# Kernel optimization log

Measured on AMD Instinct MI355X. Metric: run time of the kernel, lower is better.

The kernel has to match this reference:

```python
import jax, jax.numpy as jnp
import numpy as np

NUM_HEADS = 4


def _mha_pool(seg):
    """seg: [n_seg, S, H]. First 4 channels are attention logits (softmax over S),
    rest are values split into 4 heads; returns [n_seg, H-4]."""
    n_seg, S, H = seg.shape
    attn = jax.nn.softmax(seg[:, :, :NUM_HEADS], axis=1)          # [n, S, 4]
    vals = seg[:, :, NUM_HEADS:].reshape(n_seg, S, NUM_HEADS, -1)  # [n, S, 4, hd]
    pooled = jnp.einsum('nsh,nshd->nhd', attn, vals)               # [n, 4, hd]
    return pooled.reshape(n_seg, -1)


def setup_inputs() -> dict:
    key = jax.random.key(0)
    k1, k2, k3, k4 = jax.random.split(key, 4)
    T, D, H = 131072, 2048, 260
    embeddings = jax.random.normal(k1, (T, D), dtype=jnp.float32)
    labels = jax.random.randint(k2, (T,), 0, 2, dtype=jnp.int32)
    W_down = jax.random.normal(k3, (D, H), dtype=jnp.float32) / np.sqrt(D)
    b_down = jnp.zeros((H,), dtype=jnp.float32)
    W_final = jax.random.normal(k4, (H - NUM_HEADS, 1), dtype=jnp.float32) / np.sqrt(H - NUM_HEADS)
    b_final = jnp.zeros((1,), dtype=jnp.float32)
    return {
        'embeddings': embeddings,
        'W_down': W_down,
        'b_down': b_down,
        'W_final': W_final,
        'b_final': b_final,
        'labels': labels,
        'tokens_per_problem': 512,
        'tokens_per_line': 16,
    }


def reference(embeddings, W_down, b_down, W_final, b_final, labels,
              tokens_per_problem, tokens_per_line):
    T, D = embeddings.shape
    H = W_down.shape[1]
    # Dropout is identity in eval mode (reference baseline).
    proj = embeddings @ W_down + b_down                      # [T, H]
    # MHA_POOL_4_HEADS: keep attention logits raw, GELU (exact erf) the values.
    act = jnp.concatenate(
        [proj[:, :NUM_HEADS], jax.nn.gelu(proj[:, NUM_HEADS:], approximate=False)],
        axis=1)                                              # [T, H]

    P = T // tokens_per_problem
    problem_feat = _mha_pool(act.reshape(P, tokens_per_problem, H))   # [P, H-4]
    problem_logits = (problem_feat @ W_final + b_final)[:, 0]

    L = T // tokens_per_line
    line_feat = _mha_pool(act.reshape(L, tokens_per_line, H))         # [L, H-4]
    line_logits = (line_feat @ W_final + b_final)[:, 0]

    token_logits = (act[:, NUM_HEADS:] @ W_final + b_final)[:, 0]     # [T]

    problem_labels = labels.reshape(P, tokens_per_problem).min(axis=1)
    line_labels = labels.reshape(L, tokens_per_line).min(axis=1)
    return token_logits, line_logits, line_labels, problem_logits, problem_labels
```

## Files before the change

kernel.cpp:

```cpp
#include <hip/hip_runtime.h>
#include <hip/hip_bf16.h>
#include <math.h>

#define T_TOK   131072
#define D_IN    2048
#define H_CH    260
#define NFRAG   17
#define KSTEPS  64
#define STEP_BYTES  (NFRAG * 64 * 16)
#define CHUNK_BYTES (2 * STEP_BYTES)
#define NCHUNK  32

typedef __attribute__((ext_vector_type(8))) short bf16x8;
typedef __attribute__((ext_vector_type(4))) float f32x4;

__device__ inline short f2bf(float x) {
    __hip_bfloat16 h = __float2bfloat16(x);
    return __builtin_bit_cast(short, h);
}

__global__ void prep_wfrag(const float* __restrict__ W, __hip_bfloat16* __restrict__ Wf) {
    int g = blockIdx.x;
    int s = g / NFRAG, f = g % NFRAG;
    int lane = threadIdx.x;
    int k0 = s * 32 + (lane >> 4) * 8;
    int col = f * 16 + (lane & 15);
    short vals8[8];
#pragma unroll
    for (int j = 0; j < 8; j++) {
        float v = (col < H_CH) ? W[(size_t)(k0 + j) * H_CH + col] : 0.f;
        vals8[j] = f2bf(v);
    }
    *reinterpret_cast<bf16x8*>(reinterpret_cast<short*>(Wf) + ((size_t)g * 64 + lane) * 8) =
        *reinterpret_cast<bf16x8*>(vals8);
}

__global__ __launch_bounds__(512, 4)
void gemm_act(const float* __restrict__ emb, const __hip_bfloat16* __restrict__ Wfrag,
              const float* __restrict__ b_down, const float* __restrict__ W_final,
              const float* __restrict__ b_final,
              float* __restrict__ attnL, __hip_bfloat16* __restrict__ vals,
              float* __restrict__ token_logits) {
    __shared__ __align__(16) char smem[2 * CHUNK_BYTES];

    int wave = threadIdx.x >> 6;
    int lane = threadIdx.x & 63;
    int r0 = blockIdx.x * 128 + wave * 16;
    int row_in = lane & 15;
    int kbase = (lane >> 4) * 8;

    const char* gW = (const char*)Wfrag;

    auto stage_chunk = [&](int c, char* lbase) {
        const char* src = gW + (size_t)c * CHUNK_BYTES;
#pragma unroll
        for (int r = 0; r < 4; ++r) {
            int off = (r * 8 + wave) * 1024;
            __builtin_amdgcn_global_load_lds(
                (const __attribute__((address_space(1))) unsigned int*)(src + off + lane * 16),
                (__attribute__((address_space(3))) unsigned int*)(lbase + off), 16, 0, 0);
        }
        if (wave < 2) {
            int off = (32 + wave) * 1024;
            __builtin_amdgcn_global_load_lds(
                (const __attribute__((address_space(1))) unsigned int*)(src + off + lane * 16),
                (__attribute__((address_space(3))) unsigned int*)(lbase + off), 16, 0, 0);
        }
    };

    f32x4 acc[NFRAG];
#pragma unroll
    for (int f = 0; f < NFRAG; f++) acc[f] = (f32x4){0.f, 0.f, 0.f, 0.f};

    const float* aptr = emb + (size_t)(r0 + row_in) * D_IN + kbase;

    f32x4 P0, P1, P2, P3;
    f32x4 Q0, Q1, Q2, Q3;

    stage_chunk(0, smem);
    P0 = *reinterpret_cast<const f32x4*>(aptr);
    P1 = *reinterpret_cast<const f32x4*>(aptr + 4);
    P2 = *reinterpret_cast<const f32x4*>(aptr + 32);
    P3 = *reinterpret_cast<const f32x4*>(aptr + 36);
    __syncthreads();

#define DO_STEP(AL, AH, BOFF)                                                     \
    {                                                                             \
        bf16x8 af;                                                                \
        af[0] = f2bf(AL[0]); af[1] = f2bf(AL[1]);                                 \
        af[2] = f2bf(AL[2]); af[3] = f2bf(AL[3]);                                 \
        af[4] = f2bf(AH[0]); af[5] = f2bf(AH[1]);                                 \
        af[6] = f2bf(AH[2]); af[7] = f2bf(AH[3]);                                 \
        const char* bb = smem + (BOFF) + lane * 16;                               \
        _Pragma("unroll")                                                         \
        for (int f = 0; f < NFRAG; f++) {                                         \
            bf16x8 bfr = *reinterpret_cast<const bf16x8*>(bb + f * 1024);         \
            acc[f] = __builtin_amdgcn_mfma_f32_16x16x32_bf16(af, bfr, acc[f], 0, 0, 0); \
        }                                                                         \
    }

    for (int c = 0; c < NCHUNK; ++c) {
        int base = (c & 1) * CHUNK_BYTES;

        if (c + 1 < NCHUNK) stage_chunk(c + 1, smem + ((c + 1) & 1) * CHUNK_BYTES);
        __builtin_amdgcn_sched_barrier(0);

        int aoff = ((c + 1 < NCHUNK) ? (c + 1) * 64 : 0);
        Q0 = *reinterpret_cast<const f32x4*>(aptr + aoff);
        Q1 = *reinterpret_cast<const f32x4*>(aptr + aoff + 4);
        Q2 = *reinterpret_cast<const f32x4*>(aptr + aoff + 32);
        Q3 = *reinterpret_cast<const f32x4*>(aptr + aoff + 36);
        __builtin_amdgcn_sched_barrier(0);

        DO_STEP(P0, P1, base)
        DO_STEP(P2, P3, base + STEP_BYTES)

        asm volatile("s_waitcnt vmcnt(4) lgkmcnt(0)" ::: "memory");
        __builtin_amdgcn_s_barrier();

        P0 = Q0; P1 = Q1; P2 = Q2; P3 = Q3;
    }
#undef DO_STEP

    int colbase = lane & 15;
    int rgroup = (lane >> 4) * 4;
    float tp[4] = {0.f, 0.f, 0.f, 0.f};
#pragma unroll
    for (int f = 0; f < NFRAG; f++) {
        int n = f * 16 + colbase;
        float bias = (n < H_CH) ? b_down[n] : 0.f;
        float wf = (n >= 4 && n < H_CH) ? W_final[n - 4] : 0.f;
#pragma unroll
        for (int i = 0; i < 4; i++) {
            int row = r0 + rgroup + i;
            float v = acc[f][i] + bias;
            float a = (n < 4) ? v : 0.5f * v * (1.f + erff(v * 0.70710678118f));
            if (n < 4) {
                attnL[(size_t)row * 4 + n] = v;
            } else if (n < H_CH) {
                vals[(size_t)row * 256 + (n - 4)] = __float2bfloat16(a);
            }
            tp[i] += a * wf;
        }
    }
#pragma unroll
    for (int i = 0; i < 4; i++) {
        float v = tp[i];
        v += __shfl_xor(v, 1);
        v += __shfl_xor(v, 2);
        v += __shfl_xor(v, 4);
        v += __shfl_xor(v, 8);
        if ((lane & 15) == 0) token_logits[r0 + rgroup + i] = v + b_final[0];
    }
}

__global__ __launch_bounds__(256)
void pool_problem(const float* __restrict__ attnL, const __hip_bfloat16* __restrict__ vals,
                  const int* __restrict__ labels,
                  const float* __restrict__ W_final, const float* __restrict__ b_final,
                  float* __restrict__ out_logits, float* __restrict__ out_labels) {
    __shared__ float w_lds[512 * 4];
    __shared__ float wred[4][4];
    __shared__ float psum[4];
    __shared__ int   lred[4];

    int p = blockIdx.x;
    int t = threadIdx.x;
    int lane = t & 63, wid = t >> 6;
    const float* abase = attnL + (size_t)p * 512 * 4;

    f32x4 v0 = *reinterpret_cast<const f32x4*>(abase + (size_t)t * 4);
    f32x4 v1 = *reinterpret_cast<const f32x4*>(abase + (size_t)(t + 256) * 4);

    float mh[4];
#pragma unroll
    for (int h = 0; h < 4; h++) mh[h] = fmaxf(v0[h], v1[h]);
#pragma unroll
    for (int h = 0; h < 4; h++)
        for (int mask = 1; mask < 64; mask <<= 1) mh[h] = fmaxf(mh[h], __shfl_xor(mh[h], mask));
    if (lane == 0) {
#pragma unroll
        for (int h = 0; h < 4; h++) wred[wid][h] = mh[h];
    }
    __syncthreads();
#pragma unroll
    for (int h = 0; h < 4; h++)
        mh[h] = fmaxf(fmaxf(wred[0][h], wred[1][h]), fmaxf(wred[2][h], wred[3][h]));
    __syncthreads();

    float Zh[4];
    f32x4 e0, e1;
#pragma unroll
    for (int h = 0; h < 4; h++) {
        e0[h] = __expf(v0[h] - mh[h]);
        e1[h] = __expf(v1[h] - mh[h]);
        Zh[h] = e0[h] + e1[h];
    }
    *reinterpret_cast<f32x4*>(&w_lds[t * 4]) = e0;
    *reinterpret_cast<f32x4*>(&w_lds[(t + 256) * 4]) = e1;
#pragma unroll
    for (int h = 0; h < 4; h++)
        for (int mask = 1; mask < 64; mask <<= 1) Zh[h] += __shfl_xor(Zh[h], mask);
    if (lane == 0) {
#pragma unroll
        for (int h = 0; h < 4; h++) wred[wid][h] = Zh[h];
    }
    __syncthreads();
#pragma unroll
    for (int h = 0; h < 4; h++) Zh[h] = wred[0][h] + wred[1][h] + wred[2][h] + wred[3][h];

    int h = t >> 6;
    const __hip_bfloat16* col = vals + (size_t)p * 512 * 256 + t;
    float pooled = 0.f;
#pragma unroll 8
    for (int s = 0; s < 512; s++)
        pooled += w_lds[s * 4 + h] * __bfloat162float(col[(size_t)s * 256]);
    float part = (pooled / Zh[h]) * W_final[t];
    for (int mask = 1; mask < 64; mask <<= 1) part += __shfl_xor(part, mask);
    if (lane == 0) psum[wid] = part;

    int lmin = min(labels[p * 512 + t], labels[p * 512 + t + 256]);
    for (int mask = 1; mask < 64; mask <<= 1) lmin = min(lmin, __shfl_xor(lmin, mask));
    if (lane == 0) lred[wid] = lmin;
    __syncthreads();
    if (t == 0) {
        out_logits[p] = psum[0] + psum[1] + psum[2] + psum[3] + b_final[0];
        out_labels[p] = (float)min(min(lred[0], lred[1]), min(lred[2], lred[3]));
    }
}

__global__ __launch_bounds__(256)
void pool_line(const float* __restrict__ attnL, const __hip_bfloat16* __restrict__ vals,
               const int* __restrict__ labels,
               const float* __restrict__ W_final, const float* __restrict__ b_final,
               float* __restrict__ out_logits, float* __restrict__ out_labels) {
    int wid = threadIdx.x >> 6, lane = threadIdx.x & 63;
    int line = blockIdx.x * 4 + wid;

    float x = attnL[(size_t)line * 64 + lane];
    float mm = x;
    mm = fmaxf(mm, __shfl_xor(mm, 4));
    mm = fmaxf(mm, __shfl_xor(mm, 8));
    mm = fmaxf(mm, __shfl_xor(mm, 16));
    mm = fmaxf(mm, __shfl_xor(mm, 32));
    float e = __expf(x - mm);
    float Z = e;
    Z += __shfl_xor(Z, 4);
    Z += __shfl_xor(Z, 8);
    Z += __shfl_xor(Z, 16);
    Z += __shfl_xor(Z, 32);
    float w = e / Z;

    const __hip_bfloat16* vbase = vals + (size_t)line * 16 * 256;
    float logit_part = 0.f;
#pragma unroll
    for (int j = 0; j < 4; j++) {
        float pooled = 0.f;
#pragma unroll
        for (int s = 0; s < 16; s++) {
            float ws = __shfl(w, s * 4 + j);
            pooled += ws * __bfloat162float(vbase[(size_t)s * 256 + j * 64 + lane]);
        }
        logit_part += pooled * W_final[j * 64 + lane];
    }
    for (int mask = 1; mask < 64; mask <<= 1) logit_part += __shfl_xor(logit_part, mask);

    int lab = (lane < 16) ? labels[line * 16 + lane] : 0x7fffffff;
    for (int mask = 1; mask < 64; mask <<= 1) lab = min(lab, __shfl_xor(lab, mask));

    if (lane == 0) {
        out_logits[line] = logit_part + b_final[0];
        out_labels[line] = (float)lab;
    }
}

extern "C" void kernel_launch(void* const* d_in, const int* in_sizes, int n_in,
                              void* d_out, int out_size, void* d_ws, size_t ws_size,
                              hipStream_t stream) {
    const float* emb     = (const float*)d_in[0];
    const float* W_down  = (const float*)d_in[1];
    const float* b_down  = (const float*)d_in[2];
    const float* W_final = (const float*)d_in[3];
    const float* b_final = (const float*)d_in[4];
    const int*   labels  = (const int*)d_in[5];

    float* out      = (float*)d_out;
    float* tok      = out;
    float* line_lg  = out + 131072;
    float* line_lb  = out + 139264;
    float* prob_lg  = out + 147456;
    float* prob_lb  = out + 147712;

    __hip_bfloat16* Wfrag = (__hip_bfloat16*)d_ws;
    float* attnL = (float*)((char*)d_ws + ((size_t)4 << 20));
    __hip_bfloat16* vals = (__hip_bfloat16*)((char*)d_ws + ((size_t)8 << 20));

    prep_wfrag<<<KSTEPS * NFRAG, 64, 0, stream>>>(W_down, Wfrag);
    gemm_act<<<T_TOK / 128, 512, 0, stream>>>(emb, Wfrag, b_down, W_final, b_final,
                                              attnL, vals, tok);
    pool_problem<<<256, 256, 0, stream>>>(attnL, vals, labels, W_final, b_final, prob_lg, prob_lb);
    pool_line<<<2048, 256, 0, stream>>>(attnL, vals, labels, W_final, b_final, line_lg, line_lb);
}
```

Before: 360.5 us.

## Switch GEMM to 32x32x16 MFMA tiles with 32-row waves

The projection GEMM moves from 16x16x32 bf16 MFMA with 17 column fragments to 32x32x16 MFMA with 9 fragments of 32 columns. Each wave now owns 32 rows, and the block shrinks to 4 waves of 256 threads. The B-fragment prep layout, LDS staging and A-prefetch depth are reworked to match. The goal is fewer wasted padded columns (288 vs 272 is similar), higher MFMA efficiency and more B reuse per LDS read, at the cost of a larger accumulator footprint (144 VGPRs) and lower occupancy.

```diff
diff --git a/kernel.cpp b/kernel.cpp
--- a/kernel.cpp
+++ b/kernel.cpp
@@ -5,26 +5,34 @@
 #define T_TOK   131072
 #define D_IN    2048
 #define H_CH    260
-#define NFRAG   17
-#define KSTEPS  64
-#define STEP_BYTES  (NFRAG * 64 * 16)
-#define CHUNK_BYTES (2 * STEP_BYTES)
-#define NCHUNK  32
-
-typedef __attribute__((ext_vector_type(8))) short bf16x8;
-typedef __attribute__((ext_vector_type(4))) float f32x4;
+#define NF32    9
+#define KS16    128
+#define STEP16_BYTES (NF32 * 64 * 16)
+#define CHUNK_STEPS  4
+#define CHUNK_BYTES  (CHUNK_STEPS * STEP16_BYTES)
+#define NCHUNK  (KS16 / CHUNK_STEPS)
+
+typedef __attribute__((ext_vector_type(8)))  short bf16x8;
+typedef __attribute__((ext_vector_type(4)))  float f32x4;
+typedef __attribute__((ext_vector_type(16))) float f32x16;
 
 __device__ inline short f2bf(float x) {
     __hip_bfloat16 h = __float2bfloat16(x);
     return __builtin_bit_cast(short, h);
 }
 
+__device__ inline void glds16(const void* src, void* lds_dst) {
+    __builtin_amdgcn_global_load_lds(
+        (const __attribute__((address_space(1))) unsigned int*)src,
+        (__attribute__((address_space(3))) unsigned int*)lds_dst, 16, 0, 0);
+}
+
 __global__ void prep_wfrag(const float* __restrict__ W, __hip_bfloat16* __restrict__ Wf) {
     int g = blockIdx.x;
-    int s = g / NFRAG, f = g % NFRAG;
+    int s = g / NF32, f = g % NF32;
     int lane = threadIdx.x;
-    int k0 = s * 32 + (lane >> 4) * 8;
-    int col = f * 16 + (lane & 15);
+    int k0 = s * 16 + (lane >> 5) * 8;
+    int col = f * 32 + (lane & 31);
     short vals8[8];
 #pragma unroll
     for (int j = 0; j < 8; j++) {
@@ -35,7 +43,7 @@
         *reinterpret_cast<bf16x8*>(vals8);
 }
 
-__global__ __launch_bounds__(512, 4)
+__global__ __launch_bounds__(256, 2)
 void gemm_act(const float* __restrict__ emb, const __hip_bfloat16* __restrict__ Wfrag,
               const float* __restrict__ b_down, const float* __restrict__ W_final,
               const float* __restrict__ b_final,
@@ -45,46 +53,44 @@
 
     int wave = threadIdx.x >> 6;
     int lane = threadIdx.x & 63;
-    int r0 = blockIdx.x * 128 + wave * 16;
-    int row_in = lane & 15;
-    int kbase = (lane >> 4) * 8;
+    int r0 = blockIdx.x * 128 + wave * 32;
+    int row_in = lane & 31;
+    int kbase = (lane >> 5) * 8;
+    int hi = lane >> 5;
 
     const char* gW = (const char*)Wfrag;
 
     auto stage_chunk = [&](int c, char* lbase) {
         const char* src = gW + (size_t)c * CHUNK_BYTES;
 #pragma unroll
-        for (int r = 0; r < 4; ++r) {
-            int off = (r * 8 + wave) * 1024;
-            __builtin_amdgcn_global_load_lds(
-                (const __attribute__((address_space(1))) unsigned int*)(src + off + lane * 16),
-                (__attribute__((address_space(3))) unsigned int*)(lbase + off), 16, 0, 0);
-        }
-        if (wave < 2) {
-            int off = (32 + wave) * 1024;
-            __builtin_amdgcn_global_load_lds(
-                (const __attribute__((address_space(1))) unsigned int*)(src + off + lane * 16),
-                (__attribute__((address_space(3))) unsigned int*)(lbase + off), 16, 0, 0);
+        for (int r = 0; r < 9; ++r) {
+            int off = (r * 4 + wave) * 1024;
+            glds16(src + off + lane * 16, lbase + off);
         }
     };
 
-    f32x4 acc[NFRAG];
-#pragma unroll
-    for (int f = 0; f < NFRAG; f++) acc[f] = (f32x4){0.f, 0.f, 0.f, 0.f};
+    f32x16 acc[NF32];
+#pragma unroll
+    for (int f = 0; f < NF32; f++)
+#pragma unroll
+        for (int i = 0; i < 16; i++) acc[f][i] = 0.f;
 
     const float* aptr = emb + (size_t)(r0 + row_in) * D_IN + kbase;
 
-    f32x4 P0, P1, P2, P3;
-    f32x4 Q0, Q1, Q2, Q3;
-
-    stage_chunk(0, smem);
-    P0 = *reinterpret_cast<const f32x4*>(aptr);
-    P1 = *reinterpret_cast<const f32x4*>(aptr + 4);
-    P2 = *reinterpret_cast<const f32x4*>(aptr + 32);
-    P3 = *reinterpret_cast<const f32x4*>(aptr + 36);
-    __syncthreads();
-
-#define DO_STEP(AL, AH, BOFF)                                                     \
+    f32x4 P0, P1, P2, P3, P4, P5, P6, P7;
+    f32x4 Q0, Q1, Q2, Q3, Q4, Q5, Q6, Q7;
+
+#define LOAD_A8(R, boff)                                          \
+    R##0 = *reinterpret_cast<const f32x4*>(aptr + (boff));        \
+    R##1 = *reinterpret_cast<const f32x4*>(aptr + (boff) + 4);    \
+    R##2 = *reinterpret_cast<const f32x4*>(aptr + (boff) + 16);   \
+    R##3 = *reinterpret_cast<const f32x4*>(aptr + (boff) + 20);   \
+    R##4 = *reinterpret_cast<const f32x4*>(aptr + (boff) + 32);   \
+    R##5 = *reinterpret_cast<const f32x4*>(aptr + (boff) + 36);   \
+    R##6 = *reinterpret_cast<const f32x4*>(aptr + (boff) + 48);   \
+    R##7 = *reinterpret_cast<const f32x4*>(aptr + (boff) + 52);
+
+#define DO_STEP16(AL, AH, BOFF)                                                   \
     {                                                                             \
         bf16x8 af;                                                                \
         af[0] = f2bf(AL[0]); af[1] = f2bf(AL[1]);                                 \
@@ -93,11 +99,21 @@
         af[6] = f2bf(AH[2]); af[7] = f2bf(AH[3]);                                 \
         const char* bb = smem + (BOFF) + lane * 16;                               \
         _Pragma("unroll")                                                         \
-        for (int f = 0; f < NFRAG; f++) {                                         \
+        for (int f = 0; f < NF32; f++) {                                          \
             bf16x8 bfr = *reinterpret_cast<const bf16x8*>(bb + f * 1024);         \
-            acc[f] = __builtin_amdgcn_mfma_f32_16x16x32_bf16(af, bfr, acc[f], 0, 0, 0); \
+            acc[f] = __builtin_amdgcn_mfma_f32_32x32x16_bf16(af, bfr, acc[f], 0, 0, 0); \
         }                                                                         \
     }
+
+#define DO_CHUNK(R, base)                                   \
+    DO_STEP16(R##0, R##1, (base));                          \
+    DO_STEP16(R##2, R##3, (base) + STEP16_BYTES);           \
+    DO_STEP16(R##4, R##5, (base) + 2 * STEP16_BYTES);       \
+    DO_STEP16(R##6, R##7, (base) + 3 * STEP16_BYTES);
+
+    stage_chunk(0, smem);
+    LOAD_A8(P, 0)
+    __syncthreads();
 
     for (int c = 0; c < NCHUNK; ++c) {
         int base = (c & 1) * CHUNK_BYTES;
@@ -106,52 +122,68 @@
         __builtin_amdgcn_sched_barrier(0);
 
         int aoff = ((c + 1 < NCHUNK) ? (c + 1) * 64 : 0);
-        Q0 = *reinterpret_cast<const f32x4*>(aptr + aoff);
-        Q1 = *reinterpret_cast<const f32x4*>(aptr + aoff + 4);
-        Q2 = *reinterpret_cast<const f32x4*>(aptr + aoff + 32);
-        Q3 = *reinterpret_cast<const f32x4*>(aptr + aoff + 36);
+        LOAD_A8(Q, aoff)
         __builtin_amdgcn_sched_barrier(0);
 
-        DO_STEP(P0, P1, base)
-        DO_STEP(P2, P3, base + STEP_BYTES)
-
-        asm volatile("s_waitcnt vmcnt(4) lgkmcnt(0)" ::: "memory");
+        DO_CHUNK(P, base)
+
+        asm volatile("s_waitcnt vmcnt(8) lgkmcnt(0)" ::: "memory");
         __builtin_amdgcn_s_barrier();
 
         P0 = Q0; P1 = Q1; P2 = Q2; P3 = Q3;
-    }
-#undef DO_STEP
-
-    int colbase = lane & 15;
-    int rgroup = (lane >> 4) * 4;
-    float tp[4] = {0.f, 0.f, 0.f, 0.f};
-#pragma unroll
-    for (int f = 0; f < NFRAG; f++) {
-        int n = f * 16 + colbase;
+        P4 = Q4; P5 = Q5; P6 = Q6; P7 = Q7;
+    }
+#undef DO_CHUNK
+#undef DO_STEP16
+#undef LOAD_A8
+
+    int colbase = lane & 31;
+    float tp0, tp1, tp2, tp3, tp4, tp5, tp6, tp7;
+    float tp8, tp9, tp10, tp11, tp12, tp13, tp14, tp15;
+    tp0=tp1=tp2=tp3=tp4=tp5=tp6=tp7=0.f;
+    tp8=tp9=tp10=tp11=tp12=tp13=tp14=tp15=0.f;
+#pragma unroll
+    for (int f = 0; f < NF32; f++) {
+        int n = f * 32 + colbase;
         float bias = (n < H_CH) ? b_down[n] : 0.f;
         float wf = (n >= 4 && n < H_CH) ? W_final[n - 4] : 0.f;
 #pragma unroll
-        for (int i = 0; i < 4; i++) {
-            int row = r0 + rgroup + i;
-            float v = acc[f][i] + bias;
+        for (int r = 0; r < 16; r++) {
+            int row = r0 + (r & 3) + 8 * (r >> 2) + 4 * hi;
+            float v = acc[f][r] + bias;
             float a = (n < 4) ? v : 0.5f * v * (1.f + erff(v * 0.70710678118f));
             if (n < 4) {
                 attnL[(size_t)row * 4 + n] = v;
             } else if (n < H_CH) {
                 vals[(size_t)row * 256 + (n - 4)] = __float2bfloat16(a);
             }
-            tp[i] += a * wf;
+            float contrib = a * wf;
+            switch (r) {
+                case 0: tp0 += contrib; break;   case 1: tp1 += contrib; break;
+                case 2: tp2 += contrib; break;   case 3: tp3 += contrib; break;
+                case 4: tp4 += contrib; break;   case 5: tp5 += contrib; break;
+                case 6: tp6 += contrib; break;   case 7: tp7 += contrib; break;
+                case 8: tp8 += contrib; break;   case 9: tp9 += contrib; break;
+                case 10: tp10 += contrib; break; case 11: tp11 += contrib; break;
+                case 12: tp12 += contrib; break; case 13: tp13 += contrib; break;
+                case 14: tp14 += contrib; break; case 15: tp15 += contrib; break;
+            }
         }
     }
-#pragma unroll
-    for (int i = 0; i < 4; i++) {
-        float v = tp[i];
-        v += __shfl_xor(v, 1);
-        v += __shfl_xor(v, 2);
-        v += __shfl_xor(v, 4);
-        v += __shfl_xor(v, 8);
-        if ((lane & 15) == 0) token_logits[r0 + rgroup + i] = v + b_final[0];
-    }
+#define TOK_REDUCE(r, v)                                                      \
+    {                                                                         \
+        float x_ = (v);                                                       \
+        x_ += __shfl_xor(x_, 1);  x_ += __shfl_xor(x_, 2);                    \
+        x_ += __shfl_xor(x_, 4);  x_ += __shfl_xor(x_, 8);                    \
+        x_ += __shfl_xor(x_, 16);                                             \
+        if ((lane & 31) == 0)                                                 \
+            token_logits[r0 + ((r) & 3) + 8 * ((r) >> 2) + 4 * hi] = x_ + b_final[0]; \
+    }
+    TOK_REDUCE(0, tp0)   TOK_REDUCE(1, tp1)   TOK_REDUCE(2, tp2)   TOK_REDUCE(3, tp3)
+    TOK_REDUCE(4, tp4)   TOK_REDUCE(5, tp5)   TOK_REDUCE(6, tp6)   TOK_REDUCE(7, tp7)
+    TOK_REDUCE(8, tp8)   TOK_REDUCE(9, tp9)   TOK_REDUCE(10, tp10) TOK_REDUCE(11, tp11)
+    TOK_REDUCE(12, tp12) TOK_REDUCE(13, tp13) TOK_REDUCE(14, tp14) TOK_REDUCE(15, tp15)
+#undef TOK_REDUCE
 }
 
 __global__ __launch_bounds__(256)
@@ -295,8 +327,8 @@
     float* attnL = (float*)((char*)d_ws + ((size_t)4 << 20));
     __hip_bfloat16* vals = (__hip_bfloat16*)((char*)d_ws + ((size_t)8 << 20));
 
-    prep_wfrag<<<KSTEPS * NFRAG, 64, 0, stream>>>(W_down, Wfrag);
-    gemm_act<<<T_TOK / 128, 512, 0, stream>>>(emb, Wfrag, b_down, W_final, b_final,
+    prep_wfrag<<<KS16 * NF32, 64, 0, stream>>>(W_down, Wfrag);
+    gemm_act<<<T_TOK / 128, 256, 0, stream>>>(emb, Wfrag, b_down, W_final, b_final,
                                               attnL, vals, tok);
     pool_problem<<<256, 256, 0, stream>>>(attnL, vals, labels, W_final, b_final, prob_lg, prob_lb);
     pool_line<<<2048, 256, 0, stream>>>(attnL, vals, labels, W_final, b_final, line_lg, line_lb);
```

New measurement: 385.9 us. 1.07x slower.
